# Performance work log

Hardware: AMD Instinct MI355X
Metric: run time of the kernel (lower is better)

The kernel has to match this reference:

```python
import jax, jax.numpy as jnp
import numpy as np

B, L, V, D = 1024, 1024, 20, 128
TEMP = 1.0

# --- modular-arithmetic tables (static, built once) ---
_a = np.arange(V)
# one_hot_minus: shift_matrix[u, v] = shift[(v - u) % V]
MINUS_IDX = jnp.asarray((_a[None, :] - _a[:, None]) % V)            # [V(u), V(v)]
# one_hot_multiply: M[s, a, u] = 1 iff (s * a) % V == u
MULT_OH = jnp.asarray(np.eye(V, dtype=np.float32)[(_a[:, None] * _a[None, :]) % V])  # [V, V, V]
# multiplicative inverse permutation: INV_P[k] = one_hot(k^{-1} mod V) (0 if not coprime)
_inv = np.zeros(V, dtype=np.int64)
for k in range(1, V):
    if np.gcd(k, V) == 1:
        _inv[k] = pow(k, -1, V)
INV_P = jnp.asarray(np.eye(V, dtype=np.float32)[_inv])              # [V, V]


def one_hot_argmax(x, temperature):
    soft = jax.nn.softmax(x / temperature, axis=-1)
    hard = jax.nn.one_hot(jnp.argmax(x, axis=-1), x.shape[-1], dtype=x.dtype)
    return hard + soft - jax.lax.stop_gradient(soft)  # straight-through


def one_hot_minus(inputs, shift):
    # (inputs - shift) mod V in one-hot space
    sm = shift[..., MINUS_IDX]                         # [..., V(u), V(v)]
    return jnp.einsum('...v,...uv->...u', inputs, sm)


def one_hot_multiply(inputs, scale):
    # (inputs * scale) mod V in one-hot space
    return jnp.einsum('...a,...s,sau->...u', inputs, scale, MULT_OH)


def setup_inputs() -> dict:
    key = jax.random.key(0)
    k1, k2, k3, k4 = jax.random.split(key, 4)
    idx = jax.random.randint(k1, (B, L), 0, V)
    x = jax.nn.one_hot(idx, V, dtype=jnp.float32)                    # [B, L, V]
    emb = jax.random.normal(k2, (V, D), dtype=jnp.float32) * 0.1
    W_out = jax.random.normal(k3, (D, 2 * V), dtype=jnp.float32) * 0.1
    b = jax.random.normal(k4, (2 * V,), dtype=jnp.float32) * 0.1
    return {"x": x, "emb": emb, "W_out": W_out, "b": b}


def reference(x, emb, W_out, b):
    # strictly causal: net[t] = (sum_{s<t} out_s @ emb) @ W_out + b, so carrying
    # the cumulative embedded state reproduces the padded full-length recompute
    # of the original forward() exactly.
    batch = x.shape[0]

    def step(state, x_t):  # state [B, D], x_t [B, V]
        net = state @ W_out + b                       # [B, 2V]
        loc = one_hot_argmax(net[:, :V], TEMP).astype(x_t.dtype)
        scale = one_hot_argmax(net[:, V:], TEMP).astype(x_t.dtype)
        inverse_scale = scale @ INV_P                 # multiplicative_inverse
        out_t = one_hot_multiply(one_hot_minus(x_t, loc), inverse_scale)
        return state + out_t @ emb, out_t

    init = jnp.zeros((batch, emb.shape[1]), dtype=x.dtype)
    _, ys = jax.lax.scan(step, init, jnp.swapaxes(x, 0, 1))  # scan over length
    return jnp.swapaxes(ys, 0, 1)                             # [B, L, V]
```

## Files before the change

### kernel.cpp

```cpp
#include <hip/hip_runtime.h>
#include <cfloat>

constexpr int Bn = 1024, Ln = 1024, Vn = 20, Dn = 128;
constexpr int NJ = 2 * Vn;
constexpr int TB = 32;

__device__ __forceinline__ int mod20(int v) { return v - 20 * ((v * 205) >> 12); }

template<int CTRL>
__device__ __forceinline__ float dpp_mov(float v) {
  return __int_as_float(
      __builtin_amdgcn_update_dpp(0, __float_as_int(v), CTRL, 0xF, 0xF, false));
}
template<int CTRL>
__device__ __forceinline__ float dpp_max(float v) {
  return fmaxf(v, dpp_mov<CTRL>(v));
}
__device__ __forceinline__ float max3f(float a, float b, float c) {
  return fmaxf(fmaxf(a, b), c);
}
__device__ __forceinline__ float rowmax16(float v) {
  const float a1 = dpp_max<0xB1>(v);
  const float t2 = max3f(a1, dpp_mov<0x122>(a1), dpp_mov<0x124>(a1));
  return max3f(t2, dpp_mov<0x126>(t2), dpp_mov<0x12C>(t2));
}

constexpr unsigned long long INVT =
    (1ull << 0) | (7ull << 5) | (0ull << 10) | (3ull << 15) | (9ull << 20) |
    (11ull << 25) | (17ull << 30) | (0ull << 35) | (13ull << 40) | (19ull << 45);

__global__ __launch_bounds__(64, 1) void daf_chain(
    const float* __restrict__ x, const float* __restrict__ emb,
    const float* __restrict__ W, const float* __restrict__ bvec,
    float* __restrict__ out)
{
  __shared__ float Ws[Dn * NJ];
  __shared__ float embd[Vn * Dn];
  __shared__ alignas(8) float ewd2[Vn * 64];
  __shared__ alignas(16) double st64[Dn];
  __shared__ float nets40[64];
  __shared__ alignas(16) unsigned char aidx[Ln];

  const int lane = threadIdx.x;
  const int batch = blockIdx.x;
  const int p   = lane & 15;
  const int rB  = (lane >> 4) & 1;
  const int pos = lane & 31;

  const bool own = (lane < Vn) || (lane >= 32 && lane < 32 + Vn);
  const int  jm  = (lane < 32) ? lane : (lane - 32 + Vn);
  const int  jc  = own ? jm : 0;

  for (int i = lane; i < Dn * NJ; i += 64) Ws[i] = W[i];
  for (int i = lane; i < Vn * Dn; i += 64) embd[i] = emb[i];
  const float4* xb4 = (const float4*)(x + (size_t)batch * Ln * Vn);
  for (int i = lane; i < Ln * (Vn / 4); i += 64) {
    const float4 v = xb4[i];
    const int row = i / 5, cb = (i % 5) * 4;
    if (v.x > 0.5f) aidx[row] = (unsigned char)(cb + 0);
    if (v.y > 0.5f) aidx[row] = (unsigned char)(cb + 1);
    if (v.z > 0.5f) aidx[row] = (unsigned char)(cb + 2);
    if (v.w > 0.5f) aidx[row] = (unsigned char)(cb + 3);
  }

  for (int e = lane; e < Vn * NJ; e += 64) {
    const int k = e / NJ, j = e - k * NJ;
    double acc = 0.0;
#pragma unroll 4
    for (int d = 0; d < Dn; ++d)
      acc = __builtin_fma((double)embd[k * Dn + d], (double)Ws[d * NJ + j], acc);
    int q, slot;
    if (j < 16)      { q = j;             slot = 0; }
    else if (j < 20) { q = j - 16;        slot = 1; }
    else if (j < 36) { q = 16 + (j - 20); slot = 0; }
    else             { q = 16 + (j - 36); slot = 1; }
    ewd2[k * 64 + q * 2 + slot] = (float)acc;
  }
  if ((pos & 15) >= 4)
    for (int k = 0; k < Vn; ++k) ewd2[k * 64 + pos * 2 + 1] = 0.0f;

  const int jlo = rB ? (20 + p) : p;
  float nlo = bvec[jlo];
  float nhi = (p < 4) ? bvec[jlo + 16] : -FLT_MAX;
  const double bj = (double)bvec[jc];

  float s32a = 0.0f, s32b = 0.0f;
  float* outb = out + (size_t)batch * Ln * Vn;
  const double2* st2 = (const double2*)st64;
  const float*   Wsc = Ws + jc;
  const float2*  ew2 = (const float2*)ewd2;

  for (int tb = 0; tb < Ln / TB; ++tb) {
    const uint4 tva = *(const uint4*)(aidx + tb * TB);
    const uint4 tvb = *(const uint4*)(aidx + tb * TB + 16);
    const int tk0 = __builtin_amdgcn_readfirstlane((int)tva.x);
    const int tk1 = __builtin_amdgcn_readfirstlane((int)tva.y);
    const int tk2 = __builtin_amdgcn_readfirstlane((int)tva.z);
    const int tk3 = __builtin_amdgcn_readfirstlane((int)tva.w);
    const int tk4 = __builtin_amdgcn_readfirstlane((int)tvb.x);
    const int tk5 = __builtin_amdgcn_readfirstlane((int)tvb.y);
    const int tk6 = __builtin_amdgcn_readfirstlane((int)tvb.z);
    const int tk7 = __builtin_amdgcn_readfirstlane((int)tvb.w);

    unsigned long long q0 = 0ull, q1 = 0ull, q2 = 0ull;

#pragma unroll
    for (int u = 0; u < TB; ++u) {
      const int tw = (u < 4) ? tk0 : (u < 8) ? tk1 : (u < 12) ? tk2 :
                     (u < 16) ? tk3 : (u < 20) ? tk4 : (u < 24) ? tk5 :
                     (u < 28) ? tk6 : tk7;
      const int as = (tw >> ((u & 3) * 8)) & 0xFF;

      float m = fmaxf(nlo, nhi);
      m = rowmax16(m);
      const unsigned long long bLo = __ballot(nlo == m);
      const unsigned long long bHi = __ballot(nhi == m);
      const unsigned wLoc = ((unsigned)bLo & 0xFFFFu) | (((unsigned)bHi & 0xFu) << 16);
      const unsigned wScl = ((unsigned)(bLo >> 16) & 0xFFFFu) |
                            (((unsigned)(bHi >> 16) & 0xFu) << 16);
      const int locI = (int)__builtin_ctz(wLoc);
      const int sclI = (int)__builtin_ctz(wScl);

      const int r = as + Vn - locI;
      const int inv = (sclI & 1) ? (int)((INVT >> ((sclI >> 1) * 5)) & 31ull) : 0;
      const int oidx = mod20(inv * r);

      if (u != TB - 1) {
        const float2 e = ew2[oidx * 32 + pos];
        nlo += e.x; nhi += e.y;
      }

      if (u < 12)      q0 |= (unsigned long long)(unsigned)oidx << (5 * u);
      else if (u < 24) q1 |= (unsigned long long)(unsigned)oidx << (5 * (u - 12));
      else             q2 |= (unsigned long long)(unsigned)oidx << (5 * (u - 24));
    }

    {
      const int rl   = lane >> 1;
      const int half = lane & 1;
      const unsigned long long w = (rl < 12) ? q0 : (rl < 24) ? q1 : q2;
      const int sh = 5 * ((rl < 12) ? rl : (rl < 24) ? (rl - 12) : (rl - 24));
      const int od = (int)((w >> sh) & 31ull);
      float* ob = outb + (size_t)tb * (TB * Vn) + rl * Vn + half * 10;
      const int c0 = half * 10;
#pragma unroll
      for (int c = 0; c < 10; ++c)
        ob[c] = (c0 + c == od) ? 1.0f : 0.0f;
    }

    if (tb != Ln / TB - 1) {
#pragma unroll
      for (int u = 0; u < TB; ++u) {
        const unsigned long long w = (u < 12) ? q0 : (u < 24) ? q1 : q2;
        const int sh = 5 * ((u < 12) ? u : (u < 24) ? (u - 12) : (u - 24));
        const int ou = (int)((w >> sh) & 31ull);
        s32a += embd[ou * Dn + lane];
        s32b += embd[ou * Dn + lane + 64];
      }
      if (tb & 1) {
        st64[lane]      = (double)s32a;
        st64[lane + 64] = (double)s32b;
        double a0 = 0.0, a1 = 0.0, a2 = 0.0, a3 = 0.0;
#pragma unroll
        for (int d = 0; d < Dn; d += 4) {
          const double2 sA = st2[d >> 1];
          const double2 sB = st2[(d >> 1) + 1];
          a0 = __builtin_fma(sA.x, (double)Wsc[(d + 0) * NJ], a0);
          a1 = __builtin_fma(sA.y, (double)Wsc[(d + 1) * NJ], a1);
          a2 = __builtin_fma(sB.x, (double)Wsc[(d + 2) * NJ], a2);
          a3 = __builtin_fma(sB.y, (double)Wsc[(d + 3) * NJ], a3);
        }
        if (own) nets40[jm] = (float)(((a0 + a1) + (a2 + a3)) + bj);
        nlo = nets40[rB * 20 + p];
        nhi = (p < 4) ? nets40[rB * 20 + 16 + p] : -FLT_MAX;
      }
    }
  }
}

extern "C" void kernel_launch(void* const* d_in, const int* in_sizes, int n_in,
                              void* d_out, int out_size, void* d_ws, size_t ws_size,
                              hipStream_t stream) {
  const float* x   = (const float*)d_in[0];
  const float* emb = (const float*)d_in[1];
  const float* W   = (const float*)d_in[2];
  const float* b   = (const float*)d_in[3];
  float* out = (float*)d_out;
  hipLaunchKernelGGL(daf_chain, dim3(Bn), dim3(64), 0, stream,
                     x, emb, W, b, out);
}
```

Before: 233.3 us.

## Carry logits in double precision and drop periodic state re-projection

Precomputes emb@W as double and accumulates the 40 logits in fp64 every step, removing the per-block embedding state accumulation and the periodic full D×2V matvec that resynchronised the float logits. The removed work was a large per-64-step cost in the serial chain. In exchange each step now does fp64 adds, a wider LDS load and a double-to-float conversion, and argmax ties could differ slightly from the reference. DBL_MAX is used while only cfloat is included, which likely still compiles through the HIP headers.

Measured after the change: 225.1 us. 1.04x faster.

```diff
diff --git a/kernel.cpp b/kernel.cpp
--- a/kernel.cpp
+++ b/kernel.cpp
@@ -35,10 +35,7 @@
     float* __restrict__ out)
 {
   __shared__ float Ws[Dn * NJ];
-  __shared__ float embd[Vn * Dn];
-  __shared__ alignas(8) float ewd2[Vn * 64];
-  __shared__ alignas(16) double st64[Dn];
-  __shared__ float nets40[64];
+  __shared__ alignas(16) double ewd64[Vn * 64];
   __shared__ alignas(16) unsigned char aidx[Ln];
 
   const int lane = threadIdx.x;
@@ -47,12 +44,7 @@
   const int rB  = (lane >> 4) & 1;
   const int pos = lane & 31;
 
-  const bool own = (lane < Vn) || (lane >= 32 && lane < 32 + Vn);
-  const int  jm  = (lane < 32) ? lane : (lane - 32 + Vn);
-  const int  jc  = own ? jm : 0;
-
   for (int i = lane; i < Dn * NJ; i += 64) Ws[i] = W[i];
-  for (int i = lane; i < Vn * Dn; i += 64) embd[i] = emb[i];
   const float4* xb4 = (const float4*)(x + (size_t)batch * Ln * Vn);
   for (int i = lane; i < Ln * (Vn / 4); i += 64) {
     const float4 v = xb4[i];
@@ -68,27 +60,22 @@
     double acc = 0.0;
 #pragma unroll 4
     for (int d = 0; d < Dn; ++d)
-      acc = __builtin_fma((double)embd[k * Dn + d], (double)Ws[d * NJ + j], acc);
+      acc = __builtin_fma((double)emb[k * Dn + d], (double)Ws[d * NJ + j], acc);
     int q, slot;
     if (j < 16)      { q = j;             slot = 0; }
     else if (j < 20) { q = j - 16;        slot = 1; }
     else if (j < 36) { q = 16 + (j - 20); slot = 0; }
     else             { q = 16 + (j - 36); slot = 1; }
-    ewd2[k * 64 + q * 2 + slot] = (float)acc;
+    ewd64[k * 64 + q * 2 + slot] = acc;
   }
   if ((pos & 15) >= 4)
-    for (int k = 0; k < Vn; ++k) ewd2[k * 64 + pos * 2 + 1] = 0.0f;
+    for (int k = 0; k < Vn; ++k) ewd64[k * 64 + pos * 2 + 1] = 0.0;
 
   const int jlo = rB ? (20 + p) : p;
-  float nlo = bvec[jlo];
-  float nhi = (p < 4) ? bvec[jlo + 16] : -FLT_MAX;
-  const double bj = (double)bvec[jc];
+  double nlo64 = (double)bvec[jlo];
+  double nhi64 = (p < 4) ? (double)bvec[jlo + 16] : -DBL_MAX;
 
-  float s32a = 0.0f, s32b = 0.0f;
   float* outb = out + (size_t)batch * Ln * Vn;
-  const double2* st2 = (const double2*)st64;
-  const float*   Wsc = Ws + jc;
-  const float2*  ew2 = (const float2*)ewd2;
 
   for (int tb = 0; tb < Ln / TB; ++tb) {
     const uint4 tva = *(const uint4*)(aidx + tb * TB);
@@ -111,10 +98,12 @@
                      (u < 28) ? tk6 : tk7;
       const int as = (tw >> ((u & 3) * 8)) & 0xFF;
 
-      float m = fmaxf(nlo, nhi);
+      const float klo = (float)nlo64;
+      const float khi = (float)nhi64;
+      float m = fmaxf(klo, khi);
       m = rowmax16(m);
-      const unsigned long long bLo = __ballot(nlo == m);
-      const unsigned long long bHi = __ballot(nhi == m);
+      const unsigned long long bLo = __ballot(klo == m);
+      const unsigned long long bHi = __ballot(khi == m);
       const unsigned wLoc = ((unsigned)bLo & 0xFFFFu) | (((unsigned)bHi & 0xFu) << 16);
       const unsigned wScl = ((unsigned)(bLo >> 16) & 0xFFFFu) |
                             (((unsigned)(bHi >> 16) & 0xFu) << 16);
@@ -125,9 +114,9 @@
       const int inv = (sclI & 1) ? (int)((INVT >> ((sclI >> 1) * 5)) & 31ull) : 0;
       const int oidx = mod20(inv * r);
 
-      if (u != TB - 1) {
-        const float2 e = ew2[oidx * 32 + pos];
-        nlo += e.x; nhi += e.y;
+      {
+        const double2 e = *(const double2*)(ewd64 + oidx * 64 + pos * 2);
+        nlo64 += e.x; nhi64 += e.y;
       }
 
       if (u < 12)      q0 |= (unsigned long long)(unsigned)oidx << (5 * u);
@@ -147,34 +136,6 @@
       for (int c = 0; c < 10; ++c)
         ob[c] = (c0 + c == od) ? 1.0f : 0.0f;
     }
-
-    if (tb != Ln / TB - 1) {
-#pragma unroll
-      for (int u = 0; u < TB; ++u) {
-        const unsigned long long w = (u < 12) ? q0 : (u < 24) ? q1 : q2;
-        const int sh = 5 * ((u < 12) ? u : (u < 24) ? (u - 12) : (u - 24));
-        const int ou = (int)((w >> sh) & 31ull);
-        s32a += embd[ou * Dn + lane];
-        s32b += embd[ou * Dn + lane + 64];
-      }
-      if (tb & 1) {
-        st64[lane]      = (double)s32a;
-        st64[lane + 64] = (double)s32b;
-        double a0 = 0.0, a1 = 0.0, a2 = 0.0, a3 = 0.0;
-#pragma unroll
-        for (int d = 0; d < Dn; d += 4) {
-          const double2 sA = st2[d >> 1];
-          const double2 sB = st2[(d >> 1) + 1];
-          a0 = __builtin_fma(sA.x, (double)Wsc[(d + 0) * NJ], a0);
-          a1 = __builtin_fma(sA.y, (double)Wsc[(d + 1) * NJ], a1);
-          a2 = __builtin_fma(sB.x, (double)Wsc[(d + 2) * NJ], a2);
-          a3 = __builtin_fma(sB.y, (double)Wsc[(d + 3) * NJ], a3);
-        }
-        if (own) nets40[jm] = (float)(((a0 + a1) + (a2 + a3)) + bj);
-        nlo = nets40[rB * 20 + p];
-        nhi = (p < 4) ? nets40[rB * 20 + 16 + p] : -FLT_MAX;
-      }
-    }
   }
 }
 
```
